# Kernel optimization log

Hardware: AMD Instinct MI355X
Metric: run time of the kernel (lower is better)

## Reference

```python
import jax, jax.numpy as jnp
import numpy as np

B, ND, NPR, D, H = 8, 512, 1024, 256, 8
DH = D // H
K_T, G_MIN, RHO, B_LAM, TOPK_RATIO, EDL_LAM = 4.0, 1e-4, 0.3, 0.01, 0.5, 1e-3
NEG = -1e30  # stands in for -inf in masked_fill (softmax weight is exactly 0 either way)


def setup_inputs():
    key = jax.random.key(0)
    ks = jax.random.split(key, 20)
    H_D = jax.random.normal(ks[0], (B, ND, D), jnp.float32)
    H_P = jax.random.normal(ks[1], (B, NPR, D), jnp.float32)
    mask_D = (jax.random.uniform(ks[2], (B, ND)) > 0.2).at[:, :2].set(True)
    mask_P = (jax.random.uniform(ks[3], (B, NPR)) > 0.2).at[:, :2].set(True)
    s = 0.02
    p = {
        'nig_w': s * jax.random.normal(ks[4], (D, 4), jnp.float32),
        'nig_b': jnp.zeros((4,), jnp.float32),
        'Wq': s * jax.random.normal(ks[5], (D, D), jnp.float32), 'bq': jnp.zeros((D,), jnp.float32),
        'Wk': s * jax.random.normal(ks[6], (D, D), jnp.float32), 'bk': jnp.zeros((D,), jnp.float32),
        'Wv': s * jax.random.normal(ks[7], (D, D), jnp.float32), 'bv': jnp.zeros((D,), jnp.float32),
        'Wo': s * jax.random.normal(ks[8], (D, D), jnp.float32), 'bo': jnp.zeros((D,), jnp.float32),
        'ln_g': jnp.ones((D,), jnp.float32), 'ln_b': jnp.zeros((D,), jnp.float32),
    }
    return dict(H_D=H_D, mask_D=mask_D, H_P=H_P, mask_P=mask_P, **p)


def _layernorm(x, g, b):
    m = jnp.mean(x, -1, keepdims=True)
    v = jnp.mean((x - m) ** 2, -1, keepdims=True)
    return (x - m) * jax.lax.rsqrt(v + 1e-5) * g + b


def _nig(h, w, b):
    # NIGHead: linear d->4 evidential params; s2 = predictive variance beta/(nu*(alpha-1))
    raw = h @ w + b                               # [B,N,4]
    nu = jax.nn.softplus(raw[..., 1])
    alpha = 1.0 + jax.nn.softplus(raw[..., 2])
    beta = jax.nn.softplus(raw[..., 3])
    s2 = beta / (nu * (alpha - 1.0) + 1e-6)
    return raw[..., 0], nu, alpha, beta, s2


def _apply_topk(g, mask):
    # per-row variable k = floor(clamp(sum(mask)*ratio, min=1)); keep top-k of g, zero rest
    k = jnp.maximum(jnp.sum(mask, axis=1).astype(jnp.float32) * TOPK_RATIO, 1.0).astype(jnp.int32)
    ranks = jnp.argsort(jnp.argsort(-g, axis=1), axis=1)  # rank 0 = largest
    keep = ranks < k[:, None]
    return jnp.where(keep, g, 0.0) * mask.astype(g.dtype)


def _mhca(qx, kx, mask_k, log_g, Wq, bq, Wk, bk, Wv, bv, Wo, bo, ln_g, ln_b):
    Bq, Nq, Dd = qx.shape
    Nk = kx.shape[1]
    q = (qx @ Wq + bq).reshape(Bq, Nq, H, DH).transpose(0, 2, 1, 3)
    k = (kx @ Wk + bk).reshape(Bq, Nk, H, DH).transpose(0, 2, 1, 3)
    v = (kx @ Wv + bv).reshape(Bq, Nk, H, DH).transpose(0, 2, 1, 3)
    attn = jnp.einsum('bhqd,bhkd->bhqk', q, k) / jnp.sqrt(jnp.float32(DH))
    attn = jnp.where(mask_k[:, None, None, :], attn, NEG)
    if log_g is not None:
        attn = attn + log_g[:, None, None, :]
    w = jax.nn.softmax(attn, axis=-1)
    ctx = jnp.einsum('bhqk,bhkd->bhqd', w, v).transpose(0, 2, 1, 3).reshape(Bq, Nq, Dd)
    return _layernorm(ctx @ Wo + bo + qx, ln_g, ln_b)


def reference(H_D, mask_D, H_P, mask_P, nig_w, nig_b, Wq, bq, Wk, bk, Wv, bv, Wo, bo, ln_g, ln_b):
    # stage='B', k_now=None path
    _, _, aD, bD, s2_D = _nig(H_D, nig_w, nig_b)
    _, _, aP, bP, s2_P = _nig(H_P, nig_w, nig_b)
    mDf, mPf = mask_D.astype(jnp.float32), mask_P.astype(jnp.float32)
    # GateFromUncertainty: g = clamp(exp(-k*s2), g_min, 1) * mask
    g_D = _apply_topk(jnp.clip(jnp.exp(-K_T * s2_D), G_MIN, 1.0) * mDf, mask_D)
    g_P = _apply_topk(jnp.clip(jnp.exp(-K_T * s2_P), G_MIN, 1.0) * mPf, mask_P)
    log_g_D, log_g_P = jnp.log(g_D + 1e-8), jnp.log(g_P + 1e-8)
    # BudgetRegularizer: lam*(masked mean gate - rho)^2 ; EDLRegularizer: lam*mean(alpha+beta)
    budget = lambda g, mf: B_LAM * (jnp.sum(g) / (jnp.sum(mf) + 1e-8) - RHO) ** 2
    edl = lambda a, b: EDL_LAM * jnp.mean(a + b)
    loss_reg = budget(g_D, mDf) + budget(g_P, mPf) + edl(aD, bD) + edl(aP, bP)
    mha = (Wq, bq, Wk, bk, Wv, bv, Wo, bo, ln_g, ln_b)
    Xd, Xp = H_D, H_P
    Xd = _mhca(Xd, Xp, mask_P, log_g_P, *mha)
    Xp = _mhca(Xp, Xd, mask_D, log_g_D, *mha)
    return Xd, Xp, g_D, g_P, loss_reg
```

## Files before the change

### kernel.cpp

```cpp
#include <hip/hip_runtime.h>
#include <hip/hip_bf16.h>
#include <math.h>

typedef __attribute__((ext_vector_type(8))) short s8;
typedef __attribute__((ext_vector_type(8))) unsigned short us8;
typedef __attribute__((ext_vector_type(4))) unsigned short us4;
typedef __attribute__((ext_vector_type(4))) float f4;

__device__ __forceinline__ unsigned short f2bf(float f) {
    unsigned int u = __float_as_uint(f);
    unsigned int r = u + 0x7FFFu + ((u >> 16) & 1u);
    return (unsigned short)(r >> 16);
}

__device__ __forceinline__ float softplus_f(float x) {
    return (x > 0.f) ? x + log1pf(expf(-x)) : log1pf(expf(x));
}

__global__ __launch_bounds__(256) void prep_nig_kernel(
        const float* __restrict__ W0, const float* __restrict__ W1,
        const float* __restrict__ W2, const float* __restrict__ W3,
        unsigned short* __restrict__ Wt,
        const float* __restrict__ H_D, const int* __restrict__ maskD,
        const float* __restrict__ H_P, const int* __restrict__ maskP,
        const float* __restrict__ nw, const float* __restrict__ nb,
        float* __restrict__ gpreD, float* __restrict__ gpreP,
        float* __restrict__ abD, float* __restrict__ abP,
        unsigned short* __restrict__ hdb, unsigned short* __restrict__ hpb) {
    int bx = blockIdx.x;
    if (bx < 256) {
        __shared__ float t[32][33];
        int wsel = bx >> 6, tile = bx & 63;
        const float* W = wsel == 0 ? W0 : wsel == 1 ? W1 : wsel == 2 ? W2 : W3;
        unsigned short* O = Wt + wsel * 65536;
        int k0 = (tile >> 3) * 32, n0 = (tile & 7) * 32;
        int r = threadIdx.x >> 5, c = threadIdx.x & 31;
#pragma unroll
        for (int i = 0; i < 4; ++i) t[r + i * 8][c] = W[(k0 + r + i * 8) * 256 + n0 + c];
        __syncthreads();
#pragma unroll
        for (int i = 0; i < 4; ++i) O[(n0 + r + i * 8) * 256 + k0 + c] = f2bf(t[c][r + i * 8]);
        return;
    }
    int row = (bx - 256) * 4 + (threadIdx.x >> 6);
    int lane = threadIdx.x & 63;
    const float* H; const int* mask; float* gpre; float* ab; unsigned short* hb; int lr;
    if (row < 4096) { H = H_D; mask = maskD; gpre = gpreD; ab = abD; hb = hdb; lr = row; }
    else            { H = H_P; mask = maskP; gpre = gpreP; ab = abP; hb = hpb; lr = row - 4096; }
    float4 hv = *(const float4*)(H + (size_t)lr * 256 + lane * 4);
    us4 h4 = { f2bf(hv.x), f2bf(hv.y), f2bf(hv.z), f2bf(hv.w) };
    *(us4*)&hb[(size_t)lr * 256 + lane * 4] = h4;
    float4 n0v = *(const float4*)&nw[(lane * 4 + 0) * 4];
    float4 n1v = *(const float4*)&nw[(lane * 4 + 1) * 4];
    float4 n2v = *(const float4*)&nw[(lane * 4 + 2) * 4];
    float4 n3v = *(const float4*)&nw[(lane * 4 + 3) * 4];
    float a1 = hv.x * n0v.y + hv.y * n1v.y + hv.z * n2v.y + hv.w * n3v.y;
    float a2 = hv.x * n0v.z + hv.y * n1v.z + hv.z * n2v.z + hv.w * n3v.z;
    float a3 = hv.x * n0v.w + hv.y * n1v.w + hv.z * n2v.w + hv.w * n3v.w;
#pragma unroll
    for (int o = 32; o; o >>= 1) {
        a1 += __shfl_xor(a1, o);
        a2 += __shfl_xor(a2, o);
        a3 += __shfl_xor(a3, o);
    }
    if (lane == 0) {
        float nu = softplus_f(a1 + nb[1]);
        float sa = softplus_f(a2 + nb[2]);
        float beta = softplus_f(a3 + nb[3]);
        float s2 = beta / (nu * sa + 1e-6f);
        float g = expf(-4.f * s2);
        g = fminf(fmaxf(g, 1e-4f), 1.f);
        gpre[lr] = (mask[lr] != 0) ? g : 0.f;
        ab[lr] = (1.f + sa) + beta;
    }
}

__device__ __forceinline__ void gemm64x128_lds(
        const unsigned short* __restrict__ Ab, const unsigned short* __restrict__ Wp,
        const float* __restrict__ bias, unsigned short* __restrict__ Cb,
        int idx, unsigned short (*bpan)[5120]) {
    const int tid = threadIdx.x, wid = tid >> 6, lane = tid & 63;
    const int g = lane >> 4, lo = lane & 15;
    const size_t row0 = (size_t)(idx >> 1) * 64 + wid * 16;
    const int n0 = (idx & 1) * 128;
    const int c0 = tid >> 2, q0 = tid & 3;
    const unsigned short* gp0 = Wp + (size_t)(n0 + c0) * 256 + q0 * 8;
    const unsigned short* gp1 = Wp + (size_t)(n0 + c0 + 64) * 256 + q0 * 8;
    const int l0 = c0 * 40 + q0 * 8;
    const int l1 = (c0 + 64) * 40 + q0 * 8;
    const unsigned short* ap = Ab + (row0 + lo) * 256 + g * 8;

    f4 acc[8];
#pragma unroll
    for (int f = 0; f < 8; ++f) acc[f] = (f4){0.f, 0.f, 0.f, 0.f};

    *(us8*)&bpan[0][l0] = *(const us8*)gp0;
    *(us8*)&bpan[0][l1] = *(const us8*)gp1;
    s8 av = *(const s8*)ap;

    for (int t = 0; t < 8; ++t) {
        const int buf = t & 1;
        us8 pn0, pn1; s8 avn;
        if (t < 7) {
            pn0 = *(const us8*)(gp0 + (t + 1) * 32);
            pn1 = *(const us8*)(gp1 + (t + 1) * 32);
            avn = *(const s8*)(ap + (t + 1) * 32);
        }
        __syncthreads();
#pragma unroll
        for (int f = 0; f < 8; ++f) {
            s8 bfr = *(const s8*)&bpan[buf][(f * 16 + lo) * 40 + g * 8];
            acc[f] = __builtin_amdgcn_mfma_f32_16x16x32_bf16(av, bfr, acc[f], 0, 0, 0);
        }
        if (t < 7) {
            *(us8*)&bpan[buf ^ 1][l0] = pn0;
            *(us8*)&bpan[buf ^ 1][l1] = pn1;
            av = avn;
        }
    }
#pragma unroll
    for (int f = 0; f < 8; ++f) {
        int col = n0 + f * 16 + lo;
        float bv2 = bias[col];
#pragma unroll
        for (int r = 0; r < 4; ++r)
            Cb[(row0 + g * 4 + r) * 256 + col] = f2bf(acc[f][r] + bv2);
    }
}

__device__ __forceinline__ void topk_body(
        const float* __restrict__ gpre, const int* __restrict__ mask,
        float* __restrict__ gout, float* __restrict__ logg,
        float* __restrict__ sgArr, float* __restrict__ smArr,
        int N, int b, int by, int bslot, float* grow, float* red) {
    int tid = threadIdx.x;
    int j = by * 256 + tid;
    for (int i = tid; i < N; i += 256) grow[i] = gpre[b * N + i];
    float cpart = 0.f;
    for (int i = tid; i < N; i += 256) cpart += (mask[b * N + i] != 0) ? 1.f : 0.f;
    red[tid] = cpart;
    __syncthreads();
    for (int s = 128; s; s >>= 1) { if (tid < s) red[tid] += red[tid + s]; __syncthreads(); }
    float count = red[0];
    __syncthreads();
    int k = (int)fmaxf(count * 0.5f, 1.0f);
    float gj = grow[j];
    int rank = 0;
    for (int i = 0; i < N; ++i) {
        float gi = grow[i];
        rank += (gi > gj || (gi == gj && i < j)) ? 1 : 0;
    }
    float gf = (rank < k) ? gj : 0.f;
    gout[b * N + j] = gf;
    logg[b * N + j] = logf(gf + 1e-8f);
    red[tid] = gf;
    __syncthreads();
    for (int s = 128; s; s >>= 1) { if (tid < s) red[tid] += red[tid + s]; __syncthreads(); }
    if (tid == 0) sgArr[bslot] = red[0];
    __syncthreads();
    red[tid] = (mask[b * N + j] != 0) ? 1.f : 0.f;
    __syncthreads();
    for (int s = 128; s; s >>= 1) { if (tid < s) red[tid] += red[tid + s]; __syncthreads(); }
    if (tid == 0) smArr[bslot] = red[0];
}

__global__ __launch_bounds__(256) void qkv_topk_kernel(
        const unsigned short* __restrict__ hdb, const unsigned short* __restrict__ hpb,
        const unsigned short* __restrict__ Wt,
        const float* __restrict__ bq, const float* __restrict__ bk, const float* __restrict__ bv,
        unsigned short* __restrict__ q1b, unsigned short* __restrict__ k1b,
        unsigned short* __restrict__ v1b, unsigned short* __restrict__ q2b,
        const float* __restrict__ gpreD, const int* __restrict__ maskD,
        float* __restrict__ goutD, float* __restrict__ loggD,
        const float* __restrict__ gpreP, const int* __restrict__ maskP,
        float* __restrict__ goutP, float* __restrict__ loggP,
        float* __restrict__ sgD, float* __restrict__ smD,
        float* __restrict__ sgP, float* __restrict__ smP,
        const float* __restrict__ abD, const float* __restrict__ abP,
        float* __restrict__ edl2) {
    __shared__ unsigned short bpan[2][5120];
    int bx = blockIdx.x;
    int tid = threadIdx.x;
    if (bx == 944) {
        float* red = (float*)&bpan[0][0];
        float s1 = 0.f, s2 = 0.f;
        for (int i = tid; i < 4096; i += 256) s1 += abD[i];
        for (int i = tid; i < 8192; i += 256) s2 += abP[i];
        red[tid] = s1;
        __syncthreads();
        for (int s = 128; s; s >>= 1) { if (tid < s) red[tid] += red[tid + s]; __syncthreads(); }
        if (tid == 0) edl2[0] = red[0];
        __syncthreads();
        red[tid] = s2;
        __syncthreads();
        for (int s = 128; s; s >>= 1) { if (tid < s) red[tid] += red[tid + s]; __syncthreads(); }
        if (tid == 0) edl2[1] = red[0];
        return;
    }
    if (bx >= 896) {
        float* grow = (float*)&bpan[0][0];
        float* red = grow + 1024;
        int tb = bx - 896;
        int b = tb & 7, by = tb >> 3;
        if (by < 2) topk_body(gpreD, maskD, goutD, loggD, sgD, smD, 512, b, by, b * 2 + by, grow, red);
        else        topk_body(gpreP, maskP, goutP, loggP, sgP, smP, 1024, b, by - 2, b * 4 + (by - 2), grow, red);
        return;
    }
    const unsigned short* Ab; const unsigned short* Wp; const float* bias;
    unsigned short* Cb; int idx;
    if (bx < 128)      { Ab = hdb; Wp = Wt;          bias = bq; Cb = q1b; idx = bx; }
    else if (bx < 384) { Ab = hpb; Wp = Wt + 65536;  bias = bk; Cb = k1b; idx = bx - 128; }
    else if (bx < 640) { Ab = hpb; Wp = Wt + 131072; bias = bv; Cb = v1b; idx = bx - 384; }
    else               { Ab = hpb; Wp = Wt;          bias = bq; Cb = q2b; idx = bx - 640; }
    gemm64x128_lds(Ab, Wp, bias, Cb, idx, bpan);
}

__global__ __launch_bounds__(256) void kv2_mega_kernel(
        const unsigned short* __restrict__ xdb, const unsigned short* __restrict__ Wt,
        const float* __restrict__ bk, const float* __restrict__ bv,
        unsigned short* __restrict__ k2b, unsigned short* __restrict__ v2b) {
    __shared__ unsigned short bpan[2][5120];
    int bx = blockIdx.x;
    const unsigned short* Wp; const float* bias; unsigned short* Cb; int idx;
    if (bx < 128) { Wp = Wt + 65536;  bias = bk; Cb = k2b; idx = bx; }
    else          { Wp = Wt + 131072; bias = bv; Cb = v2b; idx = bx - 128; }
    gemm64x128_lds(xdb, Wp, bias, Cb, idx, bpan);
}

__global__ __launch_bounds__(64) void gemm_o_ln_kernel(
        const unsigned short* __restrict__ A, const unsigned short* __restrict__ Wt,
        const float* __restrict__ bias, const float* __restrict__ resid,
        const float* __restrict__ gam, const float* __restrict__ bet,
        float* __restrict__ Out, unsigned short* __restrict__ OutB,
        const float* __restrict__ sgD, const float* __restrict__ smD,
        const float* __restrict__ sgP, const float* __restrict__ smP,
        const float* __restrict__ edl2, float* __restrict__ lossOut) {
    const int lane = threadIdx.x;
    const int g = lane >> 4, lo = lane & 15;
    const size_t row0 = (size_t)blockIdx.x * 16;
    f4 acc[16];
#pragma unroll
    for (int f = 0; f < 16; ++f) acc[f] = (f4){0.f, 0.f, 0.f, 0.f};
    for (int k0 = 0; k0 < 256; k0 += 32) {
        s8 af = *(const s8*)&A[(row0 + lo) * 256 + k0 + g * 8];
#pragma unroll
        for (int f = 0; f < 16; ++f) {
            s8 bfr = *(const s8*)&Wt[(size_t)(f * 16 + lo) * 256 + k0 + g * 8];
            acc[f] = __builtin_amdgcn_mfma_f32_16x16x32_bf16(af, bfr, acc[f], 0, 0, 0);
        }
    }
#pragma unroll
    for (int r = 0; r < 4; ++r) {
        size_t row = row0 + g * 4 + r;
        float s = 0.f;
#pragma unroll
        for (int f = 0; f < 16; ++f) {
            int col = f * 16 + lo;
            float v = acc[f][r] + bias[col] + resid[row * 256 + col];
            acc[f][r] = v;
            s += v;
        }
#pragma unroll
        for (int o = 1; o < 16; o <<= 1) s += __shfl_xor(s, o);
        float mean = s * (1.f / 256.f);
        float vs = 0.f;
#pragma unroll
        for (int f = 0; f < 16; ++f) {
            float dx = acc[f][r] - mean;
            vs += dx * dx;
        }
#pragma unroll
        for (int o = 1; o < 16; o <<= 1) vs += __shfl_xor(vs, o);
        float inv = rsqrtf(vs * (1.f / 256.f) + 1e-5f);
#pragma unroll
        for (int f = 0; f < 16; ++f) {
            int col = f * 16 + lo;
            float y = (acc[f][r] - mean) * inv * gam[col] + bet[col];
            Out[row * 256 + col] = y;
            if (OutB) OutB[row * 256 + col] = f2bf(y);
        }
    }
    if (lossOut && blockIdx.x == 0) {
        float sgd = 0.f, smd = 0.f, sgp = 0.f, smp = 0.f;
        if (lane < 16) { sgd = sgD[lane]; smd = smD[lane]; }
        if (lane < 32) { sgp = sgP[lane]; smp = smP[lane]; }
#pragma unroll
        for (int o = 16; o; o >>= 1) { sgp += __shfl_xor(sgp, o); smp += __shfl_xor(smp, o); }
#pragma unroll
        for (int o = 8; o; o >>= 1) { sgd += __shfl_xor(sgd, o); smd += __shfl_xor(smd, o); }
        if (lane == 0) {
            float t1 = sgd / (smd + 1e-8f) - 0.3f;
            float t2 = sgp / (smp + 1e-8f) - 0.3f;
            lossOut[0] = 0.01f * (t1 * t1) + 0.01f * (t2 * t2)
                       + 1e-3f * (edl2[0] / 4096.f) + 1e-3f * (edl2[1] / 8192.f);
        }
    }
}

template <int NK>
__global__ __launch_bounds__(256) void attn_mfma_kernel(
        const unsigned short* __restrict__ qb, const unsigned short* __restrict__ kb,
        const unsigned short* __restrict__ vb, const float* __restrict__ logg,
        unsigned short* __restrict__ ctxb, int Nq) {
    __shared__ unsigned short Kf[2][2048];
    __shared__ unsigned short Vf[2][2048];
    __shared__ unsigned short Pf[4][1152];
    __shared__ float lg[2][64];
    constexpr int NT = NK / 64;

    const int tid = threadIdx.x;
    const int wid = tid >> 6, lane = tid & 63;
    const int g = lane >> 4, lo = lane & 15;
    const int b = blockIdx.y >> 3, h = blockIdx.y & 7;
    const int q0 = blockIdx.x * 64 + wid * 16;
    const size_t bq = (size_t)b * Nq, bk = (size_t)b * NK;
    const float scale = 0.17677669529663687f;

    const int kloc = tid >> 2, quad = tid & 3;
    const size_t gbase = (bk + kloc) * 256 + h * 32 + quad * 8;
    const int kfa = ((kloc >> 4) << 9) + (quad * 16 + (kloc & 15)) * 8;
    const int vkh = kloc >> 5, vgg = (kloc >> 3) & 3, vj = kloc & 7;
    const int vdh = quad >> 1, vl0 = (quad & 1) * 8;
    const int vb0 = ((vkh * 2 + vdh) << 9) + vgg * 128 + vj;

    s8 qf = *(const s8*)&qb[(bq + q0 + lo) * 256 + h * 32 + g * 8];

    f4 o0 = {0.f, 0.f, 0.f, 0.f}, o1 = {0.f, 0.f, 0.f, 0.f};
    float mrow[4] = {-3e38f, -3e38f, -3e38f, -3e38f};
    float lsum[4] = {0.f, 0.f, 0.f, 0.f};

    us8 kreg = *(const us8*)&kb[gbase];
    us8 vreg = *(const us8*)&vb[gbase];
    float lgreg = (tid < 64) ? logg[bk + tid] : 0.f;
    *(us8*)&Kf[0][kfa] = kreg;
#pragma unroll
    for (int jj = 0; jj < 8; ++jj) Vf[0][vb0 + (vl0 + jj) * 8] = vreg[jj];
    if (tid < 64) lg[0][tid] = lgreg;

    for (int t = 0; t < NT; ++t) {
        const int cur = t & 1;
        if (t + 1 < NT) {
            size_t ga = gbase + (size_t)(t + 1) * 64 * 256;
            kreg = *(const us8*)&kb[ga];
            vreg = *(const us8*)&vb[ga];
            if (tid < 64) lgreg = logg[bk + (t + 1) * 64 + tid];
        }
        __syncthreads();

        f4 sc[4];
#pragma unroll
        for (int ks = 0; ks < 4; ++ks) {
            s8 kfr = *(const s8*)&Kf[cur][(ks << 9) + lane * 8];
            f4 z = {0.f, 0.f, 0.f, 0.f};
            f4 s4 = __builtin_amdgcn_mfma_f32_16x16x32_bf16(qf, kfr, z, 0, 0, 0);
            float lga = lg[cur][ks * 16 + lo];
#pragma unroll
            for (int r = 0; r < 4; ++r) sc[ks][r] = s4[r] * scale + lga;
        }
        float vm[4];
#pragma unroll
        for (int r = 0; r < 4; ++r)
            vm[r] = fmaxf(fmaxf(sc[0][r], sc[1][r]), fmaxf(sc[2][r], sc[3][r]));
#pragma unroll
        for (int off = 1; off < 16; off <<= 1)
#pragma unroll
            for (int r = 0; r < 4; ++r) vm[r] = fmaxf(vm[r], __shfl_xor(vm[r], off));
        float al[4], ps[4];
#pragma unroll
        for (int r = 0; r < 4; ++r) {
            float mn = fmaxf(mrow[r], vm[r]);
            al[r] = __expf(mrow[r] - mn);
            mrow[r] = mn;
            ps[r] = 0.f;
        }
#pragma unroll
        for (int ks = 0; ks < 4; ++ks)
#pragma unroll
            for (int r = 0; r < 4; ++r) {
                float p = __expf(sc[ks][r] - mrow[r]);
                ps[r] += p;
                Pf[wid][(g * 4 + r) * 72 + ks * 16 + lo] = f2bf(p);
            }
#pragma unroll
        for (int off = 1; off < 16; off <<= 1)
#pragma unroll
            for (int r = 0; r < 4; ++r) ps[r] += __shfl_xor(ps[r], off);
#pragma unroll
        for (int r = 0; r < 4; ++r) {
            lsum[r] = lsum[r] * al[r] + ps[r];
            o0[r] *= al[r];
            o1[r] *= al[r];
        }
#pragma unroll
        for (int kh = 0; kh < 2; ++kh) {
            s8 pfr = *(const s8*)&Pf[wid][lo * 72 + kh * 32 + g * 8];
            s8 vf0 = *(const s8*)&Vf[cur][((kh * 2 + 0) << 9) + lane * 8];
            o0 = __builtin_amdgcn_mfma_f32_16x16x32_bf16(pfr, vf0, o0, 0, 0, 0);
            s8 vf1 = *(const s8*)&Vf[cur][((kh * 2 + 1) << 9) + lane * 8];
            o1 = __builtin_amdgcn_mfma_f32_16x16x32_bf16(pfr, vf1, o1, 0, 0, 0);
        }
        if (t + 1 < NT) {
            const int nxt = cur ^ 1;
            *(us8*)&Kf[nxt][kfa] = kreg;
#pragma unroll
            for (int jj = 0; jj < 8; ++jj) Vf[nxt][vb0 + (vl0 + jj) * 8] = vreg[jj];
            if (tid < 64) lg[nxt][tid] = lgreg;
        }
    }
#pragma unroll
    for (int r = 0; r < 4; ++r) {
        float inv = 1.f / lsum[r];
        unsigned short* cp = ctxb + (bq + q0 + g * 4 + r) * 256 + h * 32;
        cp[lo] = f2bf(o0[r] * inv);
        cp[16 + lo] = f2bf(o1[r] * inv);
    }
}

extern "C" void kernel_launch(void* const* d_in, const int* in_sizes, int n_in,
                              void* d_out, int out_size, void* d_ws, size_t ws_size,
                              hipStream_t stream) {
    (void)in_sizes; (void)n_in; (void)out_size; (void)ws_size;
    const float* H_D   = (const float*)d_in[0];
    const int*   maskD = (const int*)d_in[1];
    const float* H_P   = (const float*)d_in[2];
    const int*   maskP = (const int*)d_in[3];
    const float* nig_w = (const float*)d_in[4];
    const float* nig_b = (const float*)d_in[5];
    const float* Wq = (const float*)d_in[6];
    const float* bq = (const float*)d_in[7];
    const float* Wk = (const float*)d_in[8];
    const float* bk = (const float*)d_in[9];
    const float* Wv = (const float*)d_in[10];
    const float* bv = (const float*)d_in[11];
    const float* Wo = (const float*)d_in[12];
    const float* bo = (const float*)d_in[13];
    const float* ln_g = (const float*)d_in[14];
    const float* ln_b = (const float*)d_in[15];
    float* out = (float*)d_out;
    float* ws = (float*)d_ws;

    float* outXd = out + 0;
    float* outXp = out + 1048576;
    float* outGD = out + 3145728;
    float* outGP = out + 3149824;
    float* outLo = out + 3158016;

    float* abD   = ws;
    float* abP   = ws + 4096;
    float* sgD   = ws + 12288;
    float* smD   = ws + 12304;
    float* sgP   = ws + 12320;
    float* smP   = ws + 12352;
    float* edl2  = ws + 12384;
    float* gpreD = ws + 12416;
    float* gpreP = ws + 16512;
    float* logD  = ws + 24704;
    float* logP  = ws + 28800;
    unsigned short* ub  = (unsigned short*)(ws + 36992);
    unsigned short* Wt  = ub;
    unsigned short* q1b = ub + 262144;
    unsigned short* k1b = ub + 1310720;
    unsigned short* v1b = ub + 3407872;
    unsigned short* q2b = ub + 5505024;
    unsigned short* c1b = ub + 7602176;
    unsigned short* xdb = ub + 8650752;
    unsigned short* k2b = ub + 9699328;
    unsigned short* v2b = ub + 10747904;
    unsigned short* c2b = ub + 11796480;
    unsigned short* hdb = c1b;
    unsigned short* hpb = xdb;

    prep_nig_kernel<<<3328, 256, 0, stream>>>(Wq, Wk, Wv, Wo, Wt,
                                              H_D, maskD, H_P, maskP,
                                              nig_w, nig_b, gpreD, gpreP, abD, abP,
                                              hdb, hpb);
    qkv_topk_kernel<<<945, 256, 0, stream>>>(hdb, hpb, Wt, bq, bk, bv,
                                             q1b, k1b, v1b, q2b,
                                             gpreD, maskD, outGD, logD,
                                             gpreP, maskP, outGP, logP,
                                             sgD, smD, sgP, smP, abD, abP, edl2);
    attn_mfma_kernel<1024><<<dim3(8, 64), 256, 0, stream>>>(q1b, k1b, v1b, logP, c1b, 512);
    gemm_o_ln_kernel<<<256, 64, 0, stream>>>(c1b, Wt + 3 * 65536, bo, H_D, ln_g, ln_b,
                                             outXd, xdb, nullptr, nullptr, nullptr, nullptr,
                                             nullptr, nullptr);
    kv2_mega_kernel<<<256, 256, 0, stream>>>(xdb, Wt, bk, bv, k2b, v2b);
    attn_mfma_kernel<512><<<dim3(16, 64), 256, 0, stream>>>(q2b, k2b, v2b, logD, c2b, 1024);
    gemm_o_ln_kernel<<<512, 64, 0, stream>>>(c2b, Wt + 3 * 65536, bo, H_P, ln_g, ln_b,
                                             outXp, nullptr, sgD, smD, sgP, smP, edl2, outLo);
}
```

Before: 155.7 us.

## Stage Wo panels in LDS for output GEMM and preload A fragments

```diff
diff --git a/kernel.cpp b/kernel.cpp
--- a/kernel.cpp
+++ b/kernel.cpp
@@ -90,32 +90,34 @@
     const int l1 = (c0 + 64) * 40 + q0 * 8;
     const unsigned short* ap = Ab + (row0 + lo) * 256 + g * 8;
 
+    s8 av[8];
+#pragma unroll
+    for (int t = 0; t < 8; ++t) av[t] = *(const s8*)(ap + t * 32);
+
     f4 acc[8];
 #pragma unroll
     for (int f = 0; f < 8; ++f) acc[f] = (f4){0.f, 0.f, 0.f, 0.f};
 
     *(us8*)&bpan[0][l0] = *(const us8*)gp0;
     *(us8*)&bpan[0][l1] = *(const us8*)gp1;
-    s8 av = *(const s8*)ap;
-
+
+#pragma unroll
     for (int t = 0; t < 8; ++t) {
         const int buf = t & 1;
-        us8 pn0, pn1; s8 avn;
+        us8 pn0, pn1;
         if (t < 7) {
             pn0 = *(const us8*)(gp0 + (t + 1) * 32);
             pn1 = *(const us8*)(gp1 + (t + 1) * 32);
-            avn = *(const s8*)(ap + (t + 1) * 32);
         }
         __syncthreads();
 #pragma unroll
         for (int f = 0; f < 8; ++f) {
             s8 bfr = *(const s8*)&bpan[buf][(f * 16 + lo) * 40 + g * 8];
-            acc[f] = __builtin_amdgcn_mfma_f32_16x16x32_bf16(av, bfr, acc[f], 0, 0, 0);
+            acc[f] = __builtin_amdgcn_mfma_f32_16x16x32_bf16(av[t], bfr, acc[f], 0, 0, 0);
         }
         if (t < 7) {
             *(us8*)&bpan[buf ^ 1][l0] = pn0;
             *(us8*)&bpan[buf ^ 1][l1] = pn1;
-            av = avn;
         }
     }
 #pragma unroll
@@ -146,6 +148,7 @@
     int k = (int)fmaxf(count * 0.5f, 1.0f);
     float gj = grow[j];
     int rank = 0;
+#pragma unroll 4
     for (int i = 0; i < N; ++i) {
         float gi = grow[i];
         rank += (gi > gj || (gi == gj && i < j)) ? 1 : 0;
@@ -227,7 +230,7 @@
     gemm64x128_lds(xdb, Wp, bias, Cb, idx, bpan);
 }
 
-__global__ __launch_bounds__(64) void gemm_o_ln_kernel(
+__global__ __launch_bounds__(256) void gemm_o_ln_kernel(
         const unsigned short* __restrict__ A, const unsigned short* __restrict__ Wt,
         const float* __restrict__ bias, const float* __restrict__ resid,
         const float* __restrict__ gam, const float* __restrict__ bet,
@@ -235,18 +238,45 @@
         const float* __restrict__ sgD, const float* __restrict__ smD,
         const float* __restrict__ sgP, const float* __restrict__ smP,
         const float* __restrict__ edl2, float* __restrict__ lossOut) {
-    const int lane = threadIdx.x;
+    __shared__ unsigned short bpan[2][10240];
+    const int tid = threadIdx.x, wid = tid >> 6, lane = tid & 63;
     const int g = lane >> 4, lo = lane & 15;
-    const size_t row0 = (size_t)blockIdx.x * 16;
+    const size_t row0 = (size_t)blockIdx.x * 64 + wid * 16;
+    const unsigned short* gp = Wt + (size_t)tid * 256;
+    const int lbase = tid * 40;
+    const unsigned short* ap = A + (row0 + lo) * 256 + g * 8;
+
+    s8 av[8];
+#pragma unroll
+    for (int t = 0; t < 8; ++t) av[t] = *(const s8*)(ap + t * 32);
+
     f4 acc[16];
 #pragma unroll
     for (int f = 0; f < 16; ++f) acc[f] = (f4){0.f, 0.f, 0.f, 0.f};
-    for (int k0 = 0; k0 < 256; k0 += 32) {
-        s8 af = *(const s8*)&A[(row0 + lo) * 256 + k0 + g * 8];
+
+#pragma unroll
+    for (int c = 0; c < 4; ++c)
+        *(us8*)&bpan[0][lbase + c * 8] = *(const us8*)(gp + c * 8);
+
+#pragma unroll
+    for (int t = 0; t < 8; ++t) {
+        const int buf = t & 1;
+        us8 pn[4];
+        if (t < 7) {
+#pragma unroll
+            for (int c = 0; c < 4; ++c)
+                pn[c] = *(const us8*)(gp + (t + 1) * 32 + c * 8);
+        }
+        __syncthreads();
 #pragma unroll
         for (int f = 0; f < 16; ++f) {
-            s8 bfr = *(const s8*)&Wt[(size_t)(f * 16 + lo) * 256 + k0 + g * 8];
-            acc[f] = __builtin_amdgcn_mfma_f32_16x16x32_bf16(af, bfr, acc[f], 0, 0, 0);
+            s8 bfr = *(const s8*)&bpan[buf][(f * 16 + lo) * 40 + g * 8];
+            acc[f] = __builtin_amdgcn_mfma_f32_16x16x32_bf16(av[t], bfr, acc[f], 0, 0, 0);
+        }
+        if (t < 7) {
+#pragma unroll
+            for (int c = 0; c < 4; ++c)
+                *(us8*)&bpan[buf ^ 1][lbase + c * 8] = pn[c];
         }
     }
 #pragma unroll
@@ -280,7 +310,7 @@
             if (OutB) OutB[row * 256 + col] = f2bf(y);
         }
     }
-    if (lossOut && blockIdx.x == 0) {
+    if (lossOut && blockIdx.x == 0 && tid < 64) {
         float sgd = 0.f, smd = 0.f, sgp = 0.f, smp = 0.f;
         if (lane < 16) { sgd = sgD[lane]; smd = smD[lane]; }
         if (lane < 32) { sgp = sgP[lane]; smp = smP[lane]; }
@@ -480,11 +510,11 @@
                                              gpreP, maskP, outGP, logP,
                                              sgD, smD, sgP, smP, abD, abP, edl2);
     attn_mfma_kernel<1024><<<dim3(8, 64), 256, 0, stream>>>(q1b, k1b, v1b, logP, c1b, 512);
-    gemm_o_ln_kernel<<<256, 64, 0, stream>>>(c1b, Wt + 3 * 65536, bo, H_D, ln_g, ln_b,
+    gemm_o_ln_kernel<<<64, 256, 0, stream>>>(c1b, Wt + 3 * 65536, bo, H_D, ln_g, ln_b,
                                              outXd, xdb, nullptr, nullptr, nullptr, nullptr,
                                              nullptr, nullptr);
     kv2_mega_kernel<<<256, 256, 0, stream>>>(xdb, Wt, bk, bv, k2b, v2b);
     attn_mfma_kernel<512><<<dim3(16, 64), 256, 0, stream>>>(q2b, k2b, v2b, logD, c2b, 1024);
-    gemm_o_ln_kernel<<<512, 64, 0, stream>>>(c2b, Wt + 3 * 65536, bo, H_P, ln_g, ln_b,
-                                             outXp, nullptr, sgD, smD, sgP, smP, edl2, outLo);
-}
+    gemm_o_ln_kernel<<<128, 256, 0, stream>>>(c2b, Wt + 3 * 65536, bo, H_P, ln_g, ln_b,
+                                              outXp, nullptr, sgD, smD, sgP, smP, edl2, outLo);
+}
```

Measured after the change: 163.8 us. +5.2%, slower.

## Fuse output projection, LayerNorm and K/V projection for second attention

Applied to the files above, without the earlier changes.

```diff
diff --git a/kernel.cpp b/kernel.cpp
--- a/kernel.cpp
+++ b/kernel.cpp
@@ -215,23 +215,93 @@
     gemm64x128_lds(Ab, Wp, bias, Cb, idx, bpan);
 }
 
-__global__ __launch_bounds__(256) void kv2_mega_kernel(
-        const unsigned short* __restrict__ xdb, const unsigned short* __restrict__ Wt,
+__global__ __launch_bounds__(64) void gemm_o_ln_kv2_kernel(
+        const unsigned short* __restrict__ A, const unsigned short* __restrict__ Wt,
+        const float* __restrict__ bo, const float* __restrict__ resid,
+        const float* __restrict__ gam, const float* __restrict__ bet,
+        float* __restrict__ Out,
         const float* __restrict__ bk, const float* __restrict__ bv,
         unsigned short* __restrict__ k2b, unsigned short* __restrict__ v2b) {
-    __shared__ unsigned short bpan[2][5120];
-    int bx = blockIdx.x;
-    const unsigned short* Wp; const float* bias; unsigned short* Cb; int idx;
-    if (bx < 128) { Wp = Wt + 65536;  bias = bk; Cb = k2b; idx = bx; }
-    else          { Wp = Wt + 131072; bias = bv; Cb = v2b; idx = bx - 128; }
-    gemm64x128_lds(xdb, Wp, bias, Cb, idx, bpan);
+    __shared__ unsigned short xs[16][264];
+    const int lane = threadIdx.x;
+    const int g = lane >> 4, lo = lane & 15;
+    const size_t row0 = (size_t)blockIdx.x * 16;
+    f4 acc[16];
+#pragma unroll
+    for (int f = 0; f < 16; ++f) acc[f] = (f4){0.f, 0.f, 0.f, 0.f};
+    const unsigned short* Wo = Wt + 3 * 65536;
+    for (int k0 = 0; k0 < 256; k0 += 32) {
+        s8 af = *(const s8*)&A[(row0 + lo) * 256 + k0 + g * 8];
+#pragma unroll
+        for (int f = 0; f < 16; ++f) {
+            s8 bfr = *(const s8*)&Wo[(size_t)(f * 16 + lo) * 256 + k0 + g * 8];
+            acc[f] = __builtin_amdgcn_mfma_f32_16x16x32_bf16(af, bfr, acc[f], 0, 0, 0);
+        }
+    }
+#pragma unroll
+    for (int r = 0; r < 4; ++r) {
+        size_t row = row0 + g * 4 + r;
+        float s = 0.f;
+#pragma unroll
+        for (int f = 0; f < 16; ++f) {
+            int col = f * 16 + lo;
+            float v = acc[f][r] + bo[col] + resid[row * 256 + col];
+            acc[f][r] = v;
+            s += v;
+        }
+#pragma unroll
+        for (int o = 1; o < 16; o <<= 1) s += __shfl_xor(s, o);
+        float mean = s * (1.f / 256.f);
+        float vs = 0.f;
+#pragma unroll
+        for (int f = 0; f < 16; ++f) {
+            float dx = acc[f][r] - mean;
+            vs += dx * dx;
+        }
+#pragma unroll
+        for (int o = 1; o < 16; o <<= 1) vs += __shfl_xor(vs, o);
+        float inv = rsqrtf(vs * (1.f / 256.f) + 1e-5f);
+#pragma unroll
+        for (int f = 0; f < 16; ++f) {
+            int col = f * 16 + lo;
+            float y = (acc[f][r] - mean) * inv * gam[col] + bet[col];
+            Out[row * 256 + col] = y;
+            xs[g * 4 + r][col] = f2bf(y);
+        }
+    }
+    __syncthreads();
+#pragma unroll
+    for (int w = 0; w < 2; ++w) {
+        const unsigned short* Wp = Wt + (w ? 2 : 1) * 65536;
+        const float* bias = w ? bv : bk;
+        unsigned short* Cb = w ? v2b : k2b;
+        f4 ac2[16];
+#pragma unroll
+        for (int f = 0; f < 16; ++f) ac2[f] = (f4){0.f, 0.f, 0.f, 0.f};
+        for (int k0 = 0; k0 < 256; k0 += 32) {
+            s8 af = *(const s8*)&xs[lo][k0 + g * 8];
+#pragma unroll
+            for (int f = 0; f < 16; ++f) {
+                s8 bfr = *(const s8*)&Wp[(size_t)(f * 16 + lo) * 256 + k0 + g * 8];
+                ac2[f] = __builtin_amdgcn_mfma_f32_16x16x32_bf16(af, bfr, ac2[f], 0, 0, 0);
+            }
+        }
+#pragma unroll
+        for (int f = 0; f < 16; ++f) {
+            int col = f * 16 + lo;
+            float bv2 = bias[col];
+#pragma unroll
+            for (int r = 0; r < 4; ++r)
+                Cb[(row0 + g * 4 + r) * 256 + col] = f2bf(ac2[f][r] + bv2);
+        }
+    }
 }
 
 __global__ __launch_bounds__(64) void gemm_o_ln_kernel(
         const unsigned short* __restrict__ A, const unsigned short* __restrict__ Wt,
         const float* __restrict__ bias, const float* __restrict__ resid,
         const float* __restrict__ gam, const float* __restrict__ bet,
-        float* __restrict__ Out, unsigned short* __restrict__ OutB,
+        float* __restrict__ Out,
         const float* __restrict__ sgD, const float* __restrict__ smD,
         const float* __restrict__ sgP, const float* __restrict__ smP,
         const float* __restrict__ edl2, float* __restrict__ lossOut) {
@@ -275,9 +345,7 @@
 #pragma unroll
         for (int f = 0; f < 16; ++f) {
             int col = f * 16 + lo;
-            float y = (acc[f][r] - mean) * inv * gam[col] + bet[col];
-            Out[row * 256 + col] = y;
-            if (OutB) OutB[row * 256 + col] = f2bf(y);
+            Out[row * 256 + col] = (acc[f][r] - mean) * inv * gam[col] + bet[col];
         }
     }
     if (lossOut && blockIdx.x == 0) {
@@ -463,12 +531,11 @@
     unsigned short* v1b = ub + 3407872;
     unsigned short* q2b = ub + 5505024;
     unsigned short* c1b = ub + 7602176;
-    unsigned short* xdb = ub + 8650752;
-    unsigned short* k2b = ub + 9699328;
-    unsigned short* v2b = ub + 10747904;
-    unsigned short* c2b = ub + 11796480;
+    unsigned short* k2b = ub + 8650752;
+    unsigned short* v2b = ub + 9699328;
+    unsigned short* c2b = ub + 10747904;
     unsigned short* hdb = c1b;
-    unsigned short* hpb = xdb;
+    unsigned short* hpb = k2b;
 
     prep_nig_kernel<<<3328, 256, 0, stream>>>(Wq, Wk, Wv, Wo, Wt,
                                               H_D, maskD, H_P, maskP,
@@ -480,11 +547,9 @@
                                              gpreP, maskP, outGP, logP,
                                              sgD, smD, sgP, smP, abD, abP, edl2);
     attn_mfma_kernel<1024><<<dim3(8, 64), 256, 0, stream>>>(q1b, k1b, v1b, logP, c1b, 512);
-    gemm_o_ln_kernel<<<256, 64, 0, stream>>>(c1b, Wt + 3 * 65536, bo, H_D, ln_g, ln_b,
-                                             outXd, xdb, nullptr, nullptr, nullptr, nullptr,
-                                             nullptr, nullptr);
-    kv2_mega_kernel<<<256, 256, 0, stream>>>(xdb, Wt, bk, bv, k2b, v2b);
+    gemm_o_ln_kv2_kernel<<<256, 64, 0, stream>>>(c1b, Wt, bo, H_D, ln_g, ln_b,
+                                                 outXd, bk, bv, k2b, v2b);
     attn_mfma_kernel<512><<<dim3(16, 64), 256, 0, stream>>>(q2b, k2b, v2b, logD, c2b, 1024);
     gemm_o_ln_kernel<<<512, 64, 0, stream>>>(c2b, Wt + 3 * 65536, bo, H_P, ln_g, ln_b,
-                                             outXp, nullptr, sgD, smD, sgP, smP, edl2, outLo);
-}
+                                             outXp, sgD, smD, sgP, smP, edl2, outLo);
+}
```

Result: slower. 205.0 us (+31.7%).
